# Performance work log

Hardware: AMD Instinct MI355X
Metric: run time of the kernel (lower is better)

The kernel has to match this reference:

```python
import jax, jax.numpy as jnp
import numpy as np
from jax.ops import segment_sum

N_NODES = 100000
N_EDGES = 1600000
HIDDEN = 64
N_LAYERS = 4
N_CLASSES = 10
N_GRAPHS = 512


def setup_inputs() -> dict:
    key = jax.random.key(0)
    ks = jax.random.split(key, 9)
    x = jax.random.normal(ks[0], (N_NODES, HIDDEN), dtype=jnp.float32)
    edge_index = jax.random.randint(ks[1], (2, N_EDGES), 0, N_NODES, dtype=jnp.int32)
    batch = jnp.sort(jax.random.randint(ks[2], (N_NODES,), 0, N_GRAPHS, dtype=jnp.int32))
    s = 0.05
    W_enc = jax.random.normal(ks[3], (HIDDEN, HIDDEN), dtype=jnp.float32) * s
    b_enc = jax.random.normal(ks[4], (HIDDEN,), dtype=jnp.float32) * s
    W_conv = jax.random.normal(ks[5], (N_LAYERS, HIDDEN, HIDDEN), dtype=jnp.float32) * s
    b_conv = jax.random.normal(ks[6], (N_LAYERS, HIDDEN), dtype=jnp.float32) * s
    W_out = jax.random.normal(ks[7], (HIDDEN, N_CLASSES), dtype=jnp.float32) * s
    b_out = jax.random.normal(ks[8], (N_CLASSES,), dtype=jnp.float32) * s
    return {"x": x, "edge_index": edge_index, "batch": batch,
            "W_enc": W_enc, "b_enc": b_enc, "W_conv": W_conv, "b_conv": b_conv,
            "W_out": W_out, "b_out": b_out, "num_graphs": N_GRAPHS}


def reference(x, edge_index, batch, W_enc, b_enc, W_conv, b_conv, W_out, b_out, num_graphs):
    N = x.shape[0]
    src, dst = edge_index[0], edge_index[1]
    # atom_encoder: Linear
    h = x @ W_enc + b_enc
    # GCN symmetric normalization with self-loops (PyG GCNConv default):
    # deg counts incoming edges (dst) plus the self-loop.
    deg = segment_sum(jnp.ones_like(src, dtype=h.dtype), dst, num_segments=N) + 1.0
    deg_inv_sqrt = jax.lax.rsqrt(deg)
    deg_inv = 1.0 / deg  # self-loop norm = d^-1/2 * d^-1/2
    edge_norm = (deg_inv_sqrt[src] * deg_inv_sqrt[dst])[:, None]  # [E,1]
    for l in range(W_conv.shape[0]):
        hl = h @ W_conv[l]                          # [N,H]
        msg = hl[src] * edge_norm                   # gather + normalize [E,H]
        agg = segment_sum(msg, dst, num_segments=N) # scatter-add
        h = agg + hl * deg_inv[:, None] + b_conv[l] # self-loop + bias
        h = jax.nn.silu(h)                          # dropout p=0 / eval: identity
    # global_add_pool over graph ids
    pooled = segment_sum(h, batch, num_segments=num_graphs)  # [G,H]
    # readout: Linear + ReLU (make_mlp with hidden_layers=1)
    out = jax.nn.relu(pooled @ W_out + b_out)
    return out
```

## Files before the change

kernel.cpp:

```cpp
#include <hip/hip_runtime.h>
#include <math.h>

#define HIDDEN 64
#define N_LAYERS 4
#define N_CLASSES 10
#define N_GRAPHS 512
#define BSH 8
#define NPB 256
#define PART_K 2048
#define IDX_CAP 512

typedef _Float16 __h;
typedef __attribute__((ext_vector_type(4))) _Float16 half4;
typedef __attribute__((ext_vector_type(8))) _Float16 half8;
typedef __attribute__((ext_vector_type(4))) float f32x4;

__global__ __launch_bounds__(256) void k_histA(const int* __restrict__ dst,
                                               int* __restrict__ ghist, int E, int NB) {
    __shared__ int hist[512];
    int t = threadIdx.x;
    hist[t] = 0; hist[t + 256] = 0;
    __syncthreads();
    int base = blockIdx.x * PART_K;
    int kend = min(PART_K, E - base);
    for (int k = t; k < kend; k += 256) atomicAdd(&hist[dst[base + k] >> BSH], 1);
    __syncthreads();
    for (int j = t; j < NB; j += 256) {
        int h = hist[j];
        if (h) atomicAdd(&ghist[j], h);
    }
}

__global__ __launch_bounds__(256) void k_bucketscan(const int* __restrict__ ghist,
                                                    int* __restrict__ bucketbase,
                                                    int* __restrict__ gcur, int NB) {
    __shared__ int s[256];
    int t = threadIdx.x;
    int j0 = 2 * t, j1 = 2 * t + 1;
    int h0 = (j0 < NB) ? ghist[j0] : 0;
    int h1 = (j1 < NB) ? ghist[j1] : 0;
    s[t] = h0 + h1; __syncthreads();
    for (int o = 1; o < 256; o <<= 1) {
        int x = (t >= o) ? s[t - o] : 0;
        __syncthreads();
        s[t] += x;
        __syncthreads();
    }
    int base = (t == 0) ? 0 : s[t - 1];
    if (j0 <= NB) { bucketbase[j0] = base;      gcur[j0] = base; }
    if (j1 <= NB) { bucketbase[j1] = base + h0; gcur[j1] = base + h0; }
}

__global__ __launch_bounds__(256) void k_partition(const int* __restrict__ src,
                                                   const int* __restrict__ dst,
                                                   int* __restrict__ gcur,
                                                   int* __restrict__ packed,
                                                   int E, int NB) {
    __shared__ int hist[512];
    __shared__ int scanE[512];
    __shared__ int cur[512];
    __shared__ int delta[512];
    __shared__ int ps[256];
    __shared__ int stage[PART_K];
    __shared__ unsigned short stgj[PART_K];
    int t = threadIdx.x;
    int base = blockIdx.x * PART_K;
    int kend = min(PART_K, E - base);

    hist[t] = 0; hist[t + 256] = 0;
    __syncthreads();
    for (int k = t; k < kend; k += 256) atomicAdd(&hist[dst[base + k] >> BSH], 1);
    __syncthreads();

    int j0 = 2 * t, j1 = j0 + 1;
    int h0 = hist[j0], h1 = hist[j1];
    ps[t] = h0 + h1; __syncthreads();
    for (int o = 1; o < 256; o <<= 1) {
        int x = (t >= o) ? ps[t - o] : 0;
        __syncthreads();
        ps[t] += x;
        __syncthreads();
    }
    int bexc = (t == 0) ? 0 : ps[t - 1];
    scanE[j0] = bexc;
    scanE[j1] = bexc + h0;
    __syncthreads();

    for (int j = t; j < NB; j += 256) {
        int h = hist[j];
        int g = h ? atomicAdd(&gcur[j], h) : 0;
        delta[j] = g - scanE[j];
        cur[j]   = scanE[j];
    }
    __syncthreads();

    for (int k = t; k < kend; k += 256) {
        int d = dst[base + k], s = src[base + k];
        int j = d >> BSH;
        int pos = atomicAdd(&cur[j], 1);
        stage[pos] = (s << BSH) | (d & (NPB - 1));
        stgj[pos]  = (unsigned short)j;
    }
    __syncthreads();

    for (int i = t; i < kend; i += 256) {
        packed[i + delta[stgj[i]]] = stage[i];
    }
}

__global__ __launch_bounds__(256) void k_fill3(const int* __restrict__ packed,
                                               const int* __restrict__ bucketbase,
                                               int* __restrict__ rowptr,
                                               float* __restrict__ dis,
                                               int* __restrict__ csr_src,
                                               int N, int E) {
    __shared__ int cnt[256];
    __shared__ int rp[256];
    int j = blockIdx.x;
    int t = threadIdx.x;
    int node0 = j << BSH;
    int segb = bucketbase[j];
    int sege = bucketbase[j + 1];

    cnt[t] = 0; __syncthreads();
    for (int i = segb + t; i < sege; i += 256) atomicAdd(&cnt[packed[i] & (NPB - 1)], 1);
    __syncthreads();

    int c = cnt[t];
    rp[t] = c; __syncthreads();
    for (int o = 1; o < 256; o <<= 1) {
        int x = (t >= o) ? rp[t - o] : 0;
        __syncthreads();
        rp[t] += x;
        __syncthreads();
    }
    int node = node0 + t;
    int start = segb + rp[t] - c + node;
    if (node < N) {
        rowptr[node] = start;
        dis[node] = rsqrtf((float)c + 1.0f);
        csr_src[start] = node;
        if (node == N - 1) rowptr[N] = E + N;
    }
    __syncthreads();
    cnt[t] = start + 1;
    __syncthreads();
    for (int i = segb + t; i < sege; i += 256) {
        int v = packed[i];
        int slot = atomicAdd(&cnt[v & (NPB - 1)], 1);
        csr_src[slot] = v >> BSH;
    }
}

__global__ __launch_bounds__(256) void k_prepW(const float* __restrict__ Wconv,
                                               const float* __restrict__ Wenc,
                                               __h* __restrict__ Wh) {
    int idx = blockIdx.x * 256 + threadIdx.x;
    int l = idx >> 12;
    int kn = idx & 4095;
    int k = kn >> 6, n = kn & 63;
    int nt = n >> 4, nl = n & 15;
    int kt = k >> 5, kr = k & 31;
    int quad = kr >> 3, j = kr & 7;
    int lane = quad * 16 + nl;
    int pos = (((nt * 2 + kt) * 64 + lane) << 3) + j;
    float w = (l < N_LAYERS) ? Wconv[(size_t)l * 4096 + kn] : Wenc[kn];
    Wh[(l << 12) + pos] = (__h)w;
}

__global__ __launch_bounds__(256) void k_layer(const int* __restrict__ csr_src,
                                               const int* __restrict__ rowptr,
                                               const float* __restrict__ dis,
                                               const __h* __restrict__ G,
                                               const __h* __restrict__ Wh,
                                               const float* __restrict__ bias,
                                               const int* __restrict__ batch,
                                               __h* __restrict__ Gho,
                                               float* __restrict__ pooled,
                                               int N, int last) {
    __shared__ __attribute__((aligned(16))) __h At[2][16][72];
    __shared__ int sidx[2][IDX_CAP];
    int tid  = threadIdx.x;
    int wave = tid >> 6;
    int lane = tid & 63;
    int tile = wave >> 1;
    int half = wave & 1;
    int trow0 = blockIdx.x * 32 + tile * 16;
    int g8  = lane >> 3;
    int f8  = lane & 7;
    unsigned f8b = (unsigned)f8 * 16u;

    int rpi = trow0 + lane;
    int rpv = rowptr[rpi > N ? N : rpi];
    int beg0 = __shfl(rpv, 0);
    int endL = __shfl(rpv, 16);
    int L    = endL - beg0;
    bool fits = (L <= IDX_CAP);

    if (fits) {
        int t2 = tid & 127;
        const int* __restrict__ gsrc = csr_src + beg0;
        for (int k = t2; k < L; k += 128) sidx[tile][k] = gsrc[k];
    }
    __syncthreads();

    int i   = half * 8 + g8;
    int beg = __shfl(rpv, i);
    int end = __shfl(rpv, i + 1);
    int node = trow0 + i;

    const char* Gb = (const char*)G;
    const half8 z8 = {(__h)0.f, (__h)0.f, (__h)0.f, (__h)0.f,
                      (__h)0.f, (__h)0.f, (__h)0.f, (__h)0.f};
    half8 a = z8;
#define GLOAD(s) (*(const half8*)(Gb + ((((unsigned)(s)) << 7) + f8b)))

    if (fits) {
        const int* sp = sidx[tile];
        int e = beg - beg0, ee = end - beg0;
        for (; e + 8 <= ee; e += 8) {
            int s0 = sp[e + 0], s1 = sp[e + 1], s2 = sp[e + 2], s3 = sp[e + 3];
            int s4 = sp[e + 4], s5 = sp[e + 5], s6 = sp[e + 6], s7 = sp[e + 7];
            half8 r0 = GLOAD(s0), r1 = GLOAD(s1), r2 = GLOAD(s2), r3 = GLOAD(s3);
            half8 r4 = GLOAD(s4), r5 = GLOAD(s5), r6 = GLOAD(s6), r7 = GLOAD(s7);
            a += r0; a += r1; a += r2; a += r3;
            a += r4; a += r5; a += r6; a += r7;
        }
        if (e < ee) {
            #pragma unroll
            for (int k = 0; k < 8; ++k) {
                int ek = e + k;
                int ck = ek < ee ? ek : ee - 1;
                half8 r = GLOAD(sp[ck]);
                a += (ek < ee) ? r : z8;
            }
        }
    } else {
        int e = beg, ee = end;
        for (; e + 8 <= ee; e += 8) {
            int s0 = csr_src[e + 0], s1 = csr_src[e + 1], s2 = csr_src[e + 2], s3 = csr_src[e + 3];
            int s4 = csr_src[e + 4], s5 = csr_src[e + 5], s6 = csr_src[e + 6], s7 = csr_src[e + 7];
            half8 r0 = GLOAD(s0), r1 = GLOAD(s1), r2 = GLOAD(s2), r3 = GLOAD(s3);
            half8 r4 = GLOAD(s4), r5 = GLOAD(s5), r6 = GLOAD(s6), r7 = GLOAD(s7);
            a += r0; a += r1; a += r2; a += r3;
            a += r4; a += r5; a += r6; a += r7;
        }
        if (e < ee) {
            #pragma unroll
            for (int k = 0; k < 8; ++k) {
                int ek = e + k;
                int ck = ek < ee ? ek : ee - 1;
                half8 r = GLOAD(csr_src[ck]);
                a += (ek < ee) ? r : z8;
            }
        }
    }
#undef GLOAD

    float df = (node < N) ? dis[node] : 0.0f;
    __h dd = (__h)df;
    half8 dv = {dd, dd, dd, dd, dd, dd, dd, dd};
    a = a * dv;
    *(half8*)&At[tile][i][f8 * 8] = a;
    __syncthreads();

    int quad = lane >> 4, nl = lane & 15;
    half8 bf[4][2];
    #pragma unroll
    for (int nt = 0; nt < 4; ++nt)
        #pragma unroll
        for (int kt = 0; kt < 2; ++kt)
            bf[nt][kt] = *(const half8*)(Wh + (((nt * 2 + kt) * 64 + lane) << 3));

    half8 a0 = *(const half8*)&At[tile][nl][quad * 8];
    half8 a1 = *(const half8*)&At[tile][nl][32 + quad * 8];

    f32x4 acc[4];
    #pragma unroll
    for (int nt = 0; nt < 4; ++nt) {
        acc[nt] = (f32x4){0.f, 0.f, 0.f, 0.f};
        acc[nt] = __builtin_amdgcn_mfma_f32_16x16x32_f16(a0, bf[nt][0], acc[nt], 0, 0, 0);
        acc[nt] = __builtin_amdgcn_mfma_f32_16x16x32_f16(a1, bf[nt][1], acc[nt], 0, 0, 0);
    }

    float b[4];
    #pragma unroll
    for (int nt = 0; nt < 4; ++nt) b[nt] = bias[nt * 16 + nl];

    bool own = ((quad >> 1) == half);

    if (!last) {
        if (own) {
            #pragma unroll
            for (int reg = 0; reg < 4; ++reg) {
                int rr = trow0 + quad * 4 + reg;
                if (rr < N) {
                    float ds_ = dis[rr];
                    #pragma unroll
                    for (int nt = 0; nt < 4; ++nt) {
                        float v = acc[nt][reg] + b[nt];
                        v = v / (1.0f + expf(-v));
                        Gho[(size_t)rr * 64 + nt * 16 + nl] = (__h)(ds_ * v);
                    }
                }
            }
        }
    } else {
        if (own) {
            float run[4] = {0.f, 0.f, 0.f, 0.f};
            int cur = -1;
            #pragma unroll
            for (int reg = 0; reg < 4; ++reg) {
                int rr = trow0 + quad * 4 + reg;
                if (rr < N) {
                    int bi = batch[rr];
                    float vals[4];
                    #pragma unroll
                    for (int nt = 0; nt < 4; ++nt) {
                        float v = acc[nt][reg] + b[nt];
                        vals[nt] = v / (1.0f + expf(-v));
                    }
                    if (bi != cur) {
                        if (cur >= 0) {
                            #pragma unroll
                            for (int nt = 0; nt < 4; ++nt)
                                atomicAdd(&pooled[cur * 64 + nt * 16 + nl], run[nt]);
                        }
                        cur = bi;
                        #pragma unroll
                        for (int nt = 0; nt < 4; ++nt) run[nt] = vals[nt];
                    } else {
                        #pragma unroll
                        for (int nt = 0; nt < 4; ++nt) run[nt] += vals[nt];
                    }
                }
            }
            if (cur >= 0) {
                #pragma unroll
                for (int nt = 0; nt < 4; ++nt)
                    atomicAdd(&pooled[cur * 64 + nt * 16 + nl], run[nt]);
            }
        }
    }
}

__global__ __launch_bounds__(256) void k_gemm_mfma(const float* __restrict__ xf,
                                                   const __h* __restrict__ Wh,
                                                   const float* __restrict__ bias,
                                                   const float* __restrict__ dis,
                                                   __h* __restrict__ Gho,
                                                   int N) {
    int wave = threadIdx.x >> 6;
    int lane = threadIdx.x & 63;
    int row0 = (blockIdx.x * 4 + wave) * 32;
    if (row0 >= N) return;
    int quad = lane >> 4, nl = lane & 15;

    half8 bf[4][2];
    #pragma unroll
    for (int nt = 0; nt < 4; ++nt)
        #pragma unroll
        for (int kt = 0; kt < 2; ++kt)
            bf[nt][kt] = *(const half8*)(Wh + (((nt * 2 + kt) * 64 + lane) << 3));

    f32x4 acc[2][4];
    #pragma unroll
    for (int h = 0; h < 2; ++h) {
        int r = row0 + h * 16 + nl; if (r >= N) r = N - 1;
        const float* ap = xf + (size_t)r * 64 + quad * 8;
        float4 v0 = ((const float4*)ap)[0];
        float4 v1 = ((const float4*)ap)[1];
        float4 v2 = ((const float4*)(ap + 32))[0];
        float4 v3 = ((const float4*)(ap + 32))[1];
        half8 a0 = (half8){(__h)v0.x, (__h)v0.y, (__h)v0.z, (__h)v0.w,
                           (__h)v1.x, (__h)v1.y, (__h)v1.z, (__h)v1.w};
        half8 a1 = (half8){(__h)v2.x, (__h)v2.y, (__h)v2.z, (__h)v2.w,
                           (__h)v3.x, (__h)v3.y, (__h)v3.z, (__h)v3.w};
        #pragma unroll
        for (int nt = 0; nt < 4; ++nt) {
            acc[h][nt] = (f32x4){0.f, 0.f, 0.f, 0.f};
            acc[h][nt] = __builtin_amdgcn_mfma_f32_16x16x32_f16(a0, bf[nt][0], acc[h][nt], 0, 0, 0);
            acc[h][nt] = __builtin_amdgcn_mfma_f32_16x16x32_f16(a1, bf[nt][1], acc[h][nt], 0, 0, 0);
        }
    }

    float b[4];
    #pragma unroll
    for (int nt = 0; nt < 4; ++nt) b[nt] = bias[nt * 16 + nl];

    #pragma unroll
    for (int h = 0; h < 2; ++h) {
        #pragma unroll
        for (int reg = 0; reg < 4; ++reg) {
            int rr = row0 + h * 16 + quad * 4 + reg;
            if (rr < N) {
                float ds = dis[rr];
                #pragma unroll
                for (int nt = 0; nt < 4; ++nt) {
                    float v = acc[h][nt][reg] + b[nt];
                    Gho[(size_t)rr * 64 + nt * 16 + nl] = (__h)(ds * v);
                }
            }
        }
    }
}

__global__ __launch_bounds__(256) void k_readout(const float* __restrict__ pooled,
                                                 const float* __restrict__ Wout,
                                                 const float* __restrict__ bout,
                                                 float* __restrict__ out) {
    int idx = blockIdx.x * 256 + threadIdx.x;
    if (idx >= N_GRAPHS * N_CLASSES) return;
    int g = idx / N_CLASSES, c = idx % N_CLASSES;
    float s = bout[c];
    #pragma unroll
    for (int j = 0; j < 64; ++j) s += pooled[g * 64 + j] * Wout[j * N_CLASSES + c];
    out[idx] = fmaxf(s, 0.0f);
}

extern "C" void kernel_launch(void* const* d_in, const int* in_sizes, int n_in,
                              void* d_out, int out_size, void* d_ws, size_t ws_size,
                              hipStream_t stream) {
    const float* x      = (const float*)d_in[0];
    const int*   ei     = (const int*)d_in[1];
    const int*   batch  = (const int*)d_in[2];
    const float* W_enc  = (const float*)d_in[3];
    const float* b_enc  = (const float*)d_in[4];
    const float* W_conv = (const float*)d_in[5];
    const float* b_conv = (const float*)d_in[6];
    const float* W_out  = (const float*)d_in[7];
    const float* b_out  = (const float*)d_in[8];
    float* out = (float*)d_out;

    const int N = in_sizes[2];
    const int E = in_sizes[1] / 2;
    const int* src = ei;
    const int* dst = ei + E;
    const int NB   = (N + NPB - 1) >> BSH;
    const int NBLK = (E + PART_K - 1) / PART_K;

    char* ws = (char*)d_ws;
    size_t off = 0;
    auto alloc = [&](size_t bytes) -> char* {
        char* p = ws + off;
        off += (bytes + 255) & ~(size_t)255;
        return p;
    };
    int*   ghist      = (int*)alloc((size_t)(NB + 1) * sizeof(int));
    int*   bucketbase = (int*)alloc((size_t)(NB + 1) * sizeof(int));
    int*   gcur       = (int*)alloc((size_t)(NB + 1) * sizeof(int));
    int*   packed     = (int*)alloc((size_t)E * sizeof(int));
    int*   csr_src    = (int*)alloc((size_t)(E + N) * sizeof(int));
    int*   rowptr     = (int*)alloc((size_t)(N + 1) * sizeof(int));
    float* dis        = (float*)alloc((size_t)N * sizeof(float));
    __h*   bufA       = (__h*)alloc((size_t)N * HIDDEN * sizeof(__h));
    __h*   bufB       = (__h*)alloc((size_t)N * HIDDEN * sizeof(__h));
    __h*   Wh         = (__h*)alloc((size_t)(N_LAYERS + 1) * 4096 * sizeof(__h));
    float* pooled     = (float*)alloc((size_t)N_GRAPHS * HIDDEN * sizeof(float));
    (void)ws_size;

    hipMemsetAsync(ghist, 0, (size_t)(NB + 1) * sizeof(int), stream);
    hipMemsetAsync(pooled, 0, (size_t)N_GRAPHS * HIDDEN * sizeof(float), stream);

    k_histA     <<<NBLK, 256, 0, stream>>>(dst, ghist, E, NB);
    k_bucketscan<<<1,    256, 0, stream>>>(ghist, bucketbase, gcur, NB);
    k_partition <<<NBLK, 256, 0, stream>>>(src, dst, gcur, packed, E, NB);
    k_fill3     <<<NB,   256, 0, stream>>>(packed, bucketbase, rowptr, dis, csr_src, N, E);
    k_prepW<<<((N_LAYERS + 1) * 4096) / 256, 256, 0, stream>>>(W_conv, W_enc, Wh);

    int gb32 = (N + 127) / 128;
    k_gemm_mfma<<<gb32, 256, 0, stream>>>(x, Wh + (size_t)N_LAYERS * 4096, b_enc,
                                          dis, bufA, N);

    __h* bufs[2] = {bufA, bufB};
    int glayer = (N + 31) / 32;
    for (int l = 0; l < N_LAYERS; ++l) {
        int last = (l == N_LAYERS - 1);
        k_layer<<<glayer, 256, 0, stream>>>(csr_src, rowptr, dis, bufs[l & 1],
                                            Wh + (size_t)l * 4096,
                                            b_conv + (size_t)l * HIDDEN, batch,
                                            bufs[(l + 1) & 1], pooled, N, last);
    }

    k_readout<<<(N_GRAPHS * N_CLASSES + 255) / 256, 256, 0, stream>>>(pooled, W_out, b_out, out);
}
```

Measured before the change: 319.0 us.

## Split each node's neighbor gather across two lane groups with shuffle reduction

```diff
diff --git a/kernel.cpp b/kernel.cpp
--- a/kernel.cpp
+++ b/kernel.cpp
@@ -11,7 +11,6 @@
 #define IDX_CAP 512
 
 typedef _Float16 __h;
-typedef __attribute__((ext_vector_type(4))) _Float16 half4;
 typedef __attribute__((ext_vector_type(8))) _Float16 half8;
 typedef __attribute__((ext_vector_type(4))) float f32x4;
 
@@ -152,6 +151,15 @@
     }
 }
 
+__device__ __forceinline__ half8 shfl_xor_h8(half8 v, int m) {
+    int4 u = __builtin_bit_cast(int4, v);
+    u.x = __shfl_xor(u.x, m);
+    u.y = __shfl_xor(u.y, m);
+    u.z = __shfl_xor(u.z, m);
+    u.w = __shfl_xor(u.w, m);
+    return __builtin_bit_cast(half8, u);
+}
+
 __global__ __launch_bounds__(256) void k_prepW(const float* __restrict__ Wconv,
                                                const float* __restrict__ Wenc,
                                                __h* __restrict__ Wh) {
@@ -178,15 +186,14 @@
                                                __h* __restrict__ Gho,
                                                float* __restrict__ pooled,
                                                int N, int last) {
-    __shared__ __attribute__((aligned(16))) __h At[2][16][72];
-    __shared__ int sidx[2][IDX_CAP];
+    __shared__ __attribute__((aligned(16))) __h At[16][72];
+    __shared__ int sidx[IDX_CAP];
     int tid  = threadIdx.x;
     int wave = tid >> 6;
     int lane = tid & 63;
-    int tile = wave >> 1;
-    int half = wave & 1;
-    int trow0 = blockIdx.x * 32 + tile * 16;
-    int g8  = lane >> 3;
+    int trow0 = blockIdx.x * 16;
+    int g16 = lane >> 4;
+    int sub = (lane >> 3) & 1;
     int f8  = lane & 7;
     unsigned f8b = (unsigned)f8 * 16u;
 
@@ -198,13 +205,12 @@
     bool fits = (L <= IDX_CAP);
 
     if (fits) {
-        int t2 = tid & 127;
         const int* __restrict__ gsrc = csr_src + beg0;
-        for (int k = t2; k < L; k += 128) sidx[tile][k] = gsrc[k];
-    }
-    __syncthreads();
-
-    int i   = half * 8 + g8;
+        for (int k = tid; k < L; k += 256) sidx[k] = gsrc[k];
+    }
+    __syncthreads();
+
+    int i   = wave * 4 + g16;
     int beg = __shfl(rpv, i);
     int end = __shfl(rpv, i + 1);
     int node = trow0 + i;
@@ -216,52 +222,56 @@
 #define GLOAD(s) (*(const half8*)(Gb + ((((unsigned)(s)) << 7) + f8b)))
 
     if (fits) {
-        const int* sp = sidx[tile];
-        int e = beg - beg0, ee = end - beg0;
-        for (; e + 8 <= ee; e += 8) {
-            int s0 = sp[e + 0], s1 = sp[e + 1], s2 = sp[e + 2], s3 = sp[e + 3];
-            int s4 = sp[e + 4], s5 = sp[e + 5], s6 = sp[e + 6], s7 = sp[e + 7];
-            half8 r0 = GLOAD(s0), r1 = GLOAD(s1), r2 = GLOAD(s2), r3 = GLOAD(s3);
-            half8 r4 = GLOAD(s4), r5 = GLOAD(s5), r6 = GLOAD(s6), r7 = GLOAD(s7);
-            a += r0; a += r1; a += r2; a += r3;
-            a += r4; a += r5; a += r6; a += r7;
-        }
-        if (e < ee) {
-            #pragma unroll
-            for (int k = 0; k < 8; ++k) {
-                int ek = e + k;
-                int ck = ek < ee ? ek : ee - 1;
-                half8 r = GLOAD(sp[ck]);
-                a += (ek < ee) ? r : z8;
+        const int* sp = sidx;
+        int rb = beg - beg0, re = end - beg0;
+        for (int e = rb + sub * 8; e < re; e += 16) {
+            if (e + 8 <= re) {
+                int s0 = sp[e + 0], s1 = sp[e + 1], s2 = sp[e + 2], s3 = sp[e + 3];
+                int s4 = sp[e + 4], s5 = sp[e + 5], s6 = sp[e + 6], s7 = sp[e + 7];
+                half8 r0 = GLOAD(s0), r1 = GLOAD(s1), r2 = GLOAD(s2), r3 = GLOAD(s3);
+                half8 r4 = GLOAD(s4), r5 = GLOAD(s5), r6 = GLOAD(s6), r7 = GLOAD(s7);
+                a += r0; a += r1; a += r2; a += r3;
+                a += r4; a += r5; a += r6; a += r7;
+            } else {
+                #pragma unroll
+                for (int k = 0; k < 8; ++k) {
+                    int ek = e + k;
+                    int ck = ek < re ? ek : re - 1;
+                    half8 r = GLOAD(sp[ck]);
+                    a += (ek < re) ? r : z8;
+                }
             }
         }
     } else {
-        int e = beg, ee = end;
-        for (; e + 8 <= ee; e += 8) {
-            int s0 = csr_src[e + 0], s1 = csr_src[e + 1], s2 = csr_src[e + 2], s3 = csr_src[e + 3];
-            int s4 = csr_src[e + 4], s5 = csr_src[e + 5], s6 = csr_src[e + 6], s7 = csr_src[e + 7];
-            half8 r0 = GLOAD(s0), r1 = GLOAD(s1), r2 = GLOAD(s2), r3 = GLOAD(s3);
-            half8 r4 = GLOAD(s4), r5 = GLOAD(s5), r6 = GLOAD(s6), r7 = GLOAD(s7);
-            a += r0; a += r1; a += r2; a += r3;
-            a += r4; a += r5; a += r6; a += r7;
-        }
-        if (e < ee) {
-            #pragma unroll
-            for (int k = 0; k < 8; ++k) {
-                int ek = e + k;
-                int ck = ek < ee ? ek : ee - 1;
-                half8 r = GLOAD(csr_src[ck]);
-                a += (ek < ee) ? r : z8;
+        for (int e = beg + sub * 8; e < end; e += 16) {
+            if (e + 8 <= end) {
+                int s0 = csr_src[e + 0], s1 = csr_src[e + 1], s2 = csr_src[e + 2], s3 = csr_src[e + 3];
+                int s4 = csr_src[e + 4], s5 = csr_src[e + 5], s6 = csr_src[e + 6], s7 = csr_src[e + 7];
+                half8 r0 = GLOAD(s0), r1 = GLOAD(s1), r2 = GLOAD(s2), r3 = GLOAD(s3);
+                half8 r4 = GLOAD(s4), r5 = GLOAD(s5), r6 = GLOAD(s6), r7 = GLOAD(s7);
+                a += r0; a += r1; a += r2; a += r3;
+                a += r4; a += r5; a += r6; a += r7;
+            } else {
+                #pragma unroll
+                for (int k = 0; k < 8; ++k) {
+                    int ek = e + k;
+                    int ck = ek < end ? ek : end - 1;
+                    half8 r = GLOAD(csr_src[ck]);
+                    a += (ek < end) ? r : z8;
+                }
             }
         }
     }
 #undef GLOAD
 
-    float df = (node < N) ? dis[node] : 0.0f;
-    __h dd = (__h)df;
-    half8 dv = {dd, dd, dd, dd, dd, dd, dd, dd};
-    a = a * dv;
-    *(half8*)&At[tile][i][f8 * 8] = a;
+    a += shfl_xor_h8(a, 8);
+
+    if (sub == 0) {
+        float df = (node < N) ? dis[node] : 0.0f;
+        __h dd = (__h)df;
+        half8 dv = {dd, dd, dd, dd, dd, dd, dd, dd};
+        *(half8*)&At[i][f8 * 8] = a * dv;
+    }
     __syncthreads();
 
     int quad = lane >> 4, nl = lane & 15;
@@ -272,8 +282,8 @@
         for (int kt = 0; kt < 2; ++kt)
             bf[nt][kt] = *(const half8*)(Wh + (((nt * 2 + kt) * 64 + lane) << 3));
 
-    half8 a0 = *(const half8*)&At[tile][nl][quad * 8];
-    half8 a1 = *(const half8*)&At[tile][nl][32 + quad * 8];
+    half8 a0 = *(const half8*)&At[nl][quad * 8];
+    half8 a1 = *(const half8*)&At[nl][32 + quad * 8];
 
     f32x4 acc[4];
     #pragma unroll
@@ -287,7 +297,7 @@
     #pragma unroll
     for (int nt = 0; nt < 4; ++nt) b[nt] = bias[nt * 16 + nl];
 
-    bool own = ((quad >> 1) == half);
+    bool own = (quad == wave);
 
     if (!last) {
         if (own) {
@@ -473,7 +483,7 @@
                                           dis, bufA, N);
 
     __h* bufs[2] = {bufA, bufB};
-    int glayer = (N + 31) / 32;
+    int glayer = (N + 15) / 16;
     for (int l = 0; l < N_LAYERS; ++l) {
         int last = (l == N_LAYERS - 1);
         k_layer<<<glayer, 256, 0, stream>>>(csr_src, rowptr, dis, bufs[l & 1],
```

Result: slower. 356.4 us (+11.7%).
